# Kernel tuning notes

Hardware: AMD Instinct MI355X
Metric: run time of the kernel (lower is better)

The kernel has to match this reference:

```python
import jax, jax.numpy as jnp
import numpy as np

EPS = 1e-12  # F.normalize default eps


def _unfold(x, p):
    """im2col matching nn.Unfold(kernel_size=p, padding=p//2).
    x: (B,C,H,W) -> (B, C, p*p, H*W), kernel positions ordered row-major."""
    B, C, H, W = x.shape
    pad = p // 2
    xp = jnp.pad(x, ((0, 0), (0, 0), (pad, pad), (pad, pad)))
    shifts = [xp[:, :, i:i + H, j:j + W] for i in range(p) for j in range(p)]
    patches = jnp.stack(shifts, axis=2)  # (B,C,p*p,H,W)
    return patches.reshape(B, C, p * p, H * W)


def setup_inputs() -> dict:
    key = jax.random.key(0)
    k1, k2 = jax.random.split(key)
    B, C, H, W = 4, 128, 128, 128
    fe_lv = jax.random.normal(k1, (B, C, H, W), dtype=jnp.float32)
    fused_features = jax.random.normal(k2, (B, C, H, W), dtype=jnp.float32)
    return {"fe_lv": fe_lv, "fused_features": fused_features}


def reference(fe_lv, fused_features):
    p = 3
    B, C, H, W = fe_lv.shape
    K = p * p
    patches = _unfold(fused_features, p)          # (B,C,K,HW)
    fe_flat = fe_lv.reshape(B, C, H * W)          # (B,C,HW)

    # L2 normalize over channel dim (dim=1), clamped like F.normalize
    pn = patches / jnp.maximum(jnp.linalg.norm(patches, axis=1, keepdims=True), EPS)
    fn = fe_flat / jnp.maximum(jnp.linalg.norm(fe_flat, axis=1, keepdims=True), EPS)

    # cosine similarity per pixel over the K neighbors: (B,HW,K)
    cos = jnp.einsum('bckn,bcn->bnk', pn, fn)
    weights = jax.nn.softmax(cos, axis=-1)        # (B,HW,K)

    # weighted aggregation of (unnormalized) patches: (B,C,HW)
    refined = jnp.einsum('bnk,bckn->bcn', weights, patches)
    return refined.reshape(B, C, H, W) + fe_lv
```

## Files before the change

### kernel.cpp

```cpp
#include <hip/hip_runtime.h>
#include <math.h>

#define C_DIM 128
#define H_DIM 128
#define W_DIM 128
#define HW (H_DIM * W_DIM)
#define EPS_N 1e-12f
#define NT 512
#define NW 8
#define CPW 16
#define LD2(p) (*(const float2*)(p))

#define K1_PX 32
#define K1_NG 8
#define K1_CPG (C_DIM / K1_NG)
__global__ __launch_bounds__(256) void norms_fu(const float* __restrict__ fu,
                                                float* __restrict__ rn)
{
    __shared__ float part[K1_PX * 9];
    const int tid = threadIdx.x;
    const int px = tid & (K1_PX - 1);
    const int g = tid >> 5;
    const float* p = fu + (size_t)blockIdx.y * C_DIM * HW + (size_t)g * K1_CPG * HW
                     + blockIdx.x * K1_PX + px;
    float s = 0.f;
#pragma unroll
    for (int j = 0; j < K1_CPG; ++j) {
        const float v = p[(size_t)j * HW];
        s += v * v;
    }
    part[px * 9 + g] = s;
    __syncthreads();
    if (tid < K1_PX) {
        float t = 0.f;
#pragma unroll
        for (int gg = 0; gg < K1_NG; ++gg) t += part[tid * 9 + gg];
        rn[(size_t)blockIdx.y * HW + blockIdx.x * K1_PX + tid] =
            1.f / fmaxf(sqrtf(t), EPS_N);
    }
}

__global__ __launch_bounds__(NT) void asfr_main2(const float* __restrict__ fe,
                                                 const float* __restrict__ fu,
                                                 const float* __restrict__ rn,
                                                 float* __restrict__ out)
{
    __shared__ float part[NW][10][W_DIM];
    __shared__ float wl[9][W_DIM];
    __shared__ float n2r[3][W_DIM];

    const int tid = threadIdx.x;
    const int l   = tid & 63;
    const int wv  = tid >> 6;

    const int bid = blockIdx.x;
    const int cpx = gridDim.x >> 3;
    const int wb  = (bid & 7) * cpx + (bid >> 3);
    const int bz  = wb >> 7;
    const int row = wb & 127;

    const size_t imgbase = (size_t)bz * C_DIM * HW;
    const int c0   = wv * CPW;
    const int col0 = 2 * l;

    if (tid < 3 * W_DIM) {
        const int r = tid >> 7, c = tid & 127;
        const int nr = row + r - 1;
        float v = 1.f;
        if (nr >= 0 && nr < H_DIM) v = rn[(size_t)bz * HW + nr * W_DIM + c];
        n2r[r][c] = v;
    }

    const bool has_u = (row > 0), has_d = (row < H_DIM - 1);
    const int rup = has_u ? row - 1 : row;
    const int rdn = has_d ? row + 1 : row;

    const float* pfe = fe + imgbase + (size_t)c0 * HW + row * W_DIM + col0;
    const float* pfm = fu + imgbase + (size_t)c0 * HW + row * W_DIM + col0;
    const float* pfu = fu + imgbase + (size_t)c0 * HW + rup * W_DIM + col0;
    const float* pfd = fu + imgbase + (size_t)c0 * HW + rdn * W_DIM + col0;
    const float2 z2 = make_float2(0.f, 0.f);

    float2 dk[9];
#pragma unroll
    for (int k = 0; k < 9; ++k) dk[k] = z2;
    float2 fe2 = z2;

    auto acc3 = [&](const float2 f, const float2 v, const int r3) {
        float lft = __shfl_up(v.y, 1);   lft = (l == 0)  ? 0.f : lft;
        float rgt = __shfl_down(v.x, 1); rgt = (l == 63) ? 0.f : rgt;
        dk[r3+0].x += f.x * lft;  dk[r3+1].x += f.x * v.x;  dk[r3+2].x += f.x * v.y;
        dk[r3+0].y += f.y * v.x;  dk[r3+1].y += f.y * v.y;  dk[r3+2].y += f.y * rgt;
    };

#pragma unroll
    for (int jb = 0; jb < CPW / 2; ++jb) {
        const size_t offA = (size_t)(2 * jb) * HW;
        const size_t offB = offA + HW;
        float2 fA = LD2(pfe + offA); float2 uA = LD2(pfu + offA);
        float2 mA = LD2(pfm + offA); float2 dA = LD2(pfd + offA);
        float2 fB = LD2(pfe + offB); float2 uB = LD2(pfu + offB);
        float2 mB = LD2(pfm + offB); float2 dB = LD2(pfd + offB);
        if (!has_u) { uA = z2; uB = z2; }
        if (!has_d) { dA = z2; dB = z2; }
        fe2.x += fA.x * fA.x + fB.x * fB.x;
        fe2.y += fA.y * fA.y + fB.y * fB.y;
        acc3(fA, uA, 0); acc3(fA, mA, 3); acc3(fA, dA, 6);
        acc3(fB, uB, 0); acc3(fB, mB, 3); acc3(fB, dB, 6);
    }

#pragma unroll
    for (int k = 0; k < 9; ++k) *(float2*)&part[wv][k][col0] = dk[k];
    *(float2*)&part[wv][9][col0] = fe2;
    __syncthreads();

    if (tid < W_DIM) {
        const int px = tid;
        float dv[10];
#pragma unroll
        for (int k = 0; k < 10; ++k) {
            float s = 0.f;
#pragma unroll
            for (int w = 0; w < NW; ++w) s += part[w][k][px];
            dv[k] = s;
        }
        const float rfe = 1.f / fmaxf(sqrtf(dv[9]), EPS_N);
        float cs[9];
        float mx = -1e30f;
#pragma unroll
        for (int k = 0; k < 9; ++k) {
            const int di = k / 3, dj = k % 3;
            const int nr = row + di - 1;
            const int nc = px + dj - 1;
            const bool ok = (nr >= 0 && nr < H_DIM && nc >= 0 && nc < W_DIM);
            const int ncc = min(max(nc, 0), W_DIM - 1);
            const float cv = ok ? dv[k] * rfe * n2r[di][ncc] : 0.f;
            cs[k] = cv;
            mx = fmaxf(mx, cv);
        }
        float sum = 0.f;
#pragma unroll
        for (int k = 0; k < 9; ++k) { cs[k] = __expf(cs[k] - mx); sum += cs[k]; }
        const float is = 1.f / sum;
#pragma unroll
        for (int k = 0; k < 9; ++k) wl[k][px] = cs[k] * is;
    }
    __syncthreads();

    float2 w2[9];
#pragma unroll
    for (int k = 0; k < 9; ++k) w2[k] = *(const float2*)&wl[k][col0];

    auto agg3 = [&](float2& acc, const float2 v, const int r3) {
        float lft = __shfl_up(v.y, 1);   lft = (l == 0)  ? 0.f : lft;
        float rgt = __shfl_down(v.x, 1); rgt = (l == 63) ? 0.f : rgt;
        acc.x += w2[r3+0].x * lft  + w2[r3+1].x * v.x + w2[r3+2].x * v.y;
        acc.y += w2[r3+0].y * v.x  + w2[r3+1].y * v.y + w2[r3+2].y * rgt;
    };

    float* pout = out + imgbase + (size_t)c0 * HW + row * W_DIM + col0;
#pragma unroll
    for (int jb = 0; jb < CPW / 2; ++jb) {
        const size_t offA = (size_t)(2 * jb) * HW;
        const size_t offB = offA + HW;
        float2 fA = LD2(pfe + offA); float2 uA = LD2(pfu + offA);
        float2 mA = LD2(pfm + offA); float2 dA = LD2(pfd + offA);
        float2 fB = LD2(pfe + offB); float2 uB = LD2(pfu + offB);
        float2 mB = LD2(pfm + offB); float2 dB = LD2(pfd + offB);
        if (!has_u) { uA = z2; uB = z2; }
        if (!has_d) { dA = z2; dB = z2; }
        float2 accA = fA;
        float2 accB = fB;
        agg3(accA, uA, 0); agg3(accA, mA, 3); agg3(accA, dA, 6);
        agg3(accB, uB, 0); agg3(accB, mB, 3); agg3(accB, dB, 6);
        *(float2*)(pout + offA) = accA;
        *(float2*)(pout + offB) = accB;
    }
}

extern "C" void kernel_launch(void* const* d_in, const int* in_sizes, int n_in,
                              void* d_out, int out_size, void* d_ws, size_t ws_size,
                              hipStream_t stream) {
    const float* fe = (const float*)d_in[0];
    const float* fu = (const float*)d_in[1];
    float* out = (float*)d_out;
    float* rn = (float*)d_ws;
    const int B = in_sizes[0] / (C_DIM * HW);

    dim3 g1(HW / K1_PX, B);
    norms_fu<<<g1, 256, 0, stream>>>(fu, rn);

    dim3 g2(B * H_DIM);
    asfr_main2<<<g2, NT, 0, stream>>>(fe, fu, rn, out);
}
```

Baseline: 38.26 us.

## Split channel reduction across blocks and fuse patch norms into partial pass

Removes the separate norm kernel. A first kernel splits channels into four slices per row, each block computing partial dot products, fe norms and fu squared norms, and writes them to workspace. A second kernel sums the slice partials, derives neighbor-row inverse norms, computes the softmax weights and aggregates its channel slice. This quadruples the block count for better occupancy. In exchange it reads the inputs twice across separate kernels and adds workspace traffic for the partial sums.

```diff
diff --git a/kernel.cpp b/kernel.cpp
--- a/kernel.cpp
+++ b/kernel.cpp
@@ -6,48 +6,18 @@
 #define W_DIM 128
 #define HW (H_DIM * W_DIM)
 #define EPS_N 1e-12f
-#define NT 512
-#define NW 8
-#define CPW 16
+#define NSL 4
+#define CPS (C_DIM / NSL)
+#define CPWV 8
+#define NPL 11
+#define PS (NPL * W_DIM)
 #define LD2(p) (*(const float2*)(p))
 
-#define K1_PX 32
-#define K1_NG 8
-#define K1_CPG (C_DIM / K1_NG)
-__global__ __launch_bounds__(256) void norms_fu(const float* __restrict__ fu,
-                                                float* __restrict__ rn)
+__global__ __launch_bounds__(256) void k2_partial(const float* __restrict__ fe,
+                                                  const float* __restrict__ fu,
+                                                  float* __restrict__ pg)
 {
-    __shared__ float part[K1_PX * 9];
-    const int tid = threadIdx.x;
-    const int px = tid & (K1_PX - 1);
-    const int g = tid >> 5;
-    const float* p = fu + (size_t)blockIdx.y * C_DIM * HW + (size_t)g * K1_CPG * HW
-                     + blockIdx.x * K1_PX + px;
-    float s = 0.f;
-#pragma unroll
-    for (int j = 0; j < K1_CPG; ++j) {
-        const float v = p[(size_t)j * HW];
-        s += v * v;
-    }
-    part[px * 9 + g] = s;
-    __syncthreads();
-    if (tid < K1_PX) {
-        float t = 0.f;
-#pragma unroll
-        for (int gg = 0; gg < K1_NG; ++gg) t += part[tid * 9 + gg];
-        rn[(size_t)blockIdx.y * HW + blockIdx.x * K1_PX + tid] =
-            1.f / fmaxf(sqrtf(t), EPS_N);
-    }
-}
-
-__global__ __launch_bounds__(NT) void asfr_main2(const float* __restrict__ fe,
-                                                 const float* __restrict__ fu,
-                                                 const float* __restrict__ rn,
-                                                 float* __restrict__ out)
-{
-    __shared__ float part[NW][10][W_DIM];
-    __shared__ float wl[9][W_DIM];
-    __shared__ float n2r[3][W_DIM];
+    __shared__ float pl[4][PS];
 
     const int tid = threadIdx.x;
     const int l   = tid & 63;
@@ -56,20 +26,14 @@
     const int bid = blockIdx.x;
     const int cpx = gridDim.x >> 3;
     const int wb  = (bid & 7) * cpx + (bid >> 3);
-    const int bz  = wb >> 7;
-    const int row = wb & 127;
+    const int slice = wb & (NSL - 1);
+    const int RG  = wb >> 2;
+    const int bz  = RG >> 7;
+    const int row = RG & 127;
 
     const size_t imgbase = (size_t)bz * C_DIM * HW;
-    const int c0   = wv * CPW;
+    const int c0   = slice * CPS + wv * CPWV;
     const int col0 = 2 * l;
-
-    if (tid < 3 * W_DIM) {
-        const int r = tid >> 7, c = tid & 127;
-        const int nr = row + r - 1;
-        float v = 1.f;
-        if (nr >= 0 && nr < H_DIM) v = rn[(size_t)bz * HW + nr * W_DIM + c];
-        n2r[r][c] = v;
-    }
 
     const bool has_u = (row > 0), has_d = (row < H_DIM - 1);
     const int rup = has_u ? row - 1 : row;
@@ -84,7 +48,7 @@
     float2 dk[9];
 #pragma unroll
     for (int k = 0; k < 9; ++k) dk[k] = z2;
-    float2 fe2 = z2;
+    float2 fe2 = z2, s2 = z2;
 
     auto acc3 = [&](const float2 f, const float2 v, const int r3) {
         float lft = __shfl_up(v.y, 1);   lft = (l == 0)  ? 0.f : lft;
@@ -94,37 +58,68 @@
     };
 
 #pragma unroll
-    for (int jb = 0; jb < CPW / 2; ++jb) {
-        const size_t offA = (size_t)(2 * jb) * HW;
-        const size_t offB = offA + HW;
-        float2 fA = LD2(pfe + offA); float2 uA = LD2(pfu + offA);
-        float2 mA = LD2(pfm + offA); float2 dA = LD2(pfd + offA);
-        float2 fB = LD2(pfe + offB); float2 uB = LD2(pfu + offB);
-        float2 mB = LD2(pfm + offB); float2 dB = LD2(pfd + offB);
-        if (!has_u) { uA = z2; uB = z2; }
-        if (!has_d) { dA = z2; dB = z2; }
-        fe2.x += fA.x * fA.x + fB.x * fB.x;
-        fe2.y += fA.y * fA.y + fB.y * fB.y;
-        acc3(fA, uA, 0); acc3(fA, mA, 3); acc3(fA, dA, 6);
-        acc3(fB, uB, 0); acc3(fB, mB, 3); acc3(fB, dB, 6);
+    for (int j = 0; j < CPWV; ++j) {
+        const size_t off = (size_t)j * HW;
+        float2 f = LD2(pfe + off);
+        float2 u = LD2(pfu + off);
+        float2 m = LD2(pfm + off);
+        float2 d = LD2(pfd + off);
+        if (!has_u) u = z2;
+        if (!has_d) d = z2;
+        fe2.x += f.x * f.x; fe2.y += f.y * f.y;
+        s2.x  += m.x * m.x; s2.y  += m.y * m.y;
+        acc3(f, u, 0); acc3(f, m, 3); acc3(f, d, 6);
     }
 
 #pragma unroll
-    for (int k = 0; k < 9; ++k) *(float2*)&part[wv][k][col0] = dk[k];
-    *(float2*)&part[wv][9][col0] = fe2;
+    for (int k = 0; k < 9; ++k) *(float2*)&pl[wv][k * W_DIM + col0] = dk[k];
+    *(float2*)&pl[wv][9 * W_DIM + col0]  = fe2;
+    *(float2*)&pl[wv][10 * W_DIM + col0] = s2;
+    __syncthreads();
+
+    float* dst = pg + ((size_t)RG * NSL + slice) * PS;
+    for (int t = tid; t < PS; t += 256)
+        dst[t] = pl[0][t] + pl[1][t] + pl[2][t] + pl[3][t];
+}
+
+__global__ __launch_bounds__(256) void k3_agg(const float* __restrict__ fe,
+                                              const float* __restrict__ fu,
+                                              const float* __restrict__ pg,
+                                              float* __restrict__ out)
+{
+    __shared__ float dvs[10 * W_DIM];
+    __shared__ float n2r[3 * W_DIM];
+    __shared__ float wl[9][W_DIM];
+
+    const int tid = threadIdx.x;
+    const int l   = tid & 63;
+    const int wv  = tid >> 6;
+
+    const int bid = blockIdx.x;
+    const int cpx = gridDim.x >> 3;
+    const int wb  = (bid & 7) * cpx + (bid >> 3);
+    const int cg  = wb & (NSL - 1);
+    const int RG  = wb >> 2;
+    const int bz  = RG >> 7;
+    const int row = RG & 127;
+
+    {
+        const float* src = pg + (size_t)RG * NSL * PS;
+        for (int t = tid; t < 10 * W_DIM; t += 256)
+            dvs[t] = src[t] + src[PS + t] + src[2 * PS + t] + src[3 * PS + t];
+    }
+    for (int t = tid; t < 3 * W_DIM; t += 256) {
+        const int r = t >> 7, c = t & 127;
+        const int nrc = min(max(row + r - 1, 0), H_DIM - 1);
+        const float* nb = pg + ((size_t)(bz * H_DIM + nrc) * NSL) * PS + 10 * W_DIM;
+        const float s = nb[c] + nb[PS + c] + nb[2 * PS + c] + nb[3 * PS + c];
+        n2r[t] = 1.f / fmaxf(sqrtf(s), EPS_N);
+    }
     __syncthreads();
 
     if (tid < W_DIM) {
         const int px = tid;
-        float dv[10];
-#pragma unroll
-        for (int k = 0; k < 10; ++k) {
-            float s = 0.f;
-#pragma unroll
-            for (int w = 0; w < NW; ++w) s += part[w][k][px];
-            dv[k] = s;
-        }
-        const float rfe = 1.f / fmaxf(sqrtf(dv[9]), EPS_N);
+        const float rfe = 1.f / fmaxf(sqrtf(dvs[9 * W_DIM + px]), EPS_N);
         float cs[9];
         float mx = -1e30f;
 #pragma unroll
@@ -134,7 +129,7 @@
             const int nc = px + dj - 1;
             const bool ok = (nr >= 0 && nr < H_DIM && nc >= 0 && nc < W_DIM);
             const int ncc = min(max(nc, 0), W_DIM - 1);
-            const float cv = ok ? dv[k] * rfe * n2r[di][ncc] : 0.f;
+            const float cv = ok ? dvs[k * W_DIM + px] * rfe * n2r[di * W_DIM + ncc] : 0.f;
             cs[k] = cv;
             mx = fmaxf(mx, cv);
         }
@@ -147,6 +142,20 @@
     }
     __syncthreads();
 
+    const size_t imgbase = (size_t)bz * C_DIM * HW;
+    const int c0   = cg * CPS + wv * CPWV;
+    const int col0 = 2 * l;
+    const bool has_u = (row > 0), has_d = (row < H_DIM - 1);
+    const int rup = has_u ? row - 1 : row;
+    const int rdn = has_d ? row + 1 : row;
+
+    const float* pfe = fe + imgbase + (size_t)c0 * HW + row * W_DIM + col0;
+    const float* pfm = fu + imgbase + (size_t)c0 * HW + row * W_DIM + col0;
+    const float* pfu = fu + imgbase + (size_t)c0 * HW + rup * W_DIM + col0;
+    const float* pfd = fu + imgbase + (size_t)c0 * HW + rdn * W_DIM + col0;
+    float* pout = out + imgbase + (size_t)c0 * HW + row * W_DIM + col0;
+    const float2 z2 = make_float2(0.f, 0.f);
+
     float2 w2[9];
 #pragma unroll
     for (int k = 0; k < 9; ++k) w2[k] = *(const float2*)&wl[k][col0];
@@ -158,23 +167,18 @@
         acc.y += w2[r3+0].y * v.x  + w2[r3+1].y * v.y + w2[r3+2].y * rgt;
     };
 
-    float* pout = out + imgbase + (size_t)c0 * HW + row * W_DIM + col0;
 #pragma unroll
-    for (int jb = 0; jb < CPW / 2; ++jb) {
-        const size_t offA = (size_t)(2 * jb) * HW;
-        const size_t offB = offA + HW;
-        float2 fA = LD2(pfe + offA); float2 uA = LD2(pfu + offA);
-        float2 mA = LD2(pfm + offA); float2 dA = LD2(pfd + offA);
-        float2 fB = LD2(pfe + offB); float2 uB = LD2(pfu + offB);
-        float2 mB = LD2(pfm + offB); float2 dB = LD2(pfd + offB);
-        if (!has_u) { uA = z2; uB = z2; }
-        if (!has_d) { dA = z2; dB = z2; }
-        float2 accA = fA;
-        float2 accB = fB;
-        agg3(accA, uA, 0); agg3(accA, mA, 3); agg3(accA, dA, 6);
-        agg3(accB, uB, 0); agg3(accB, mB, 3); agg3(accB, dB, 6);
-        *(float2*)(pout + offA) = accA;
-        *(float2*)(pout + offB) = accB;
+    for (int j = 0; j < CPWV; ++j) {
+        const size_t off = (size_t)j * HW;
+        float2 f = LD2(pfe + off);
+        float2 u = LD2(pfu + off);
+        float2 m = LD2(pfm + off);
+        float2 d = LD2(pfd + off);
+        if (!has_u) u = z2;
+        if (!has_d) d = z2;
+        float2 acc = f;
+        agg3(acc, u, 0); agg3(acc, m, 3); agg3(acc, d, 6);
+        *(float2*)(pout + off) = acc;
     }
 }
 
@@ -184,12 +188,10 @@
     const float* fe = (const float*)d_in[0];
     const float* fu = (const float*)d_in[1];
     float* out = (float*)d_out;
-    float* rn = (float*)d_ws;
+    float* pg = (float*)d_ws;
     const int B = in_sizes[0] / (C_DIM * HW);
 
-    dim3 g1(HW / K1_PX, B);
-    norms_fu<<<g1, 256, 0, stream>>>(fu, rn);
-
-    dim3 g2(B * H_DIM);
-    asfr_main2<<<g2, NT, 0, stream>>>(fe, fu, rn, out);
+    dim3 g(B * H_DIM * NSL);
+    k2_partial<<<g, 256, 0, stream>>>(fe, fu, pg);
+    k3_agg<<<g, 256, 0, stream>>>(fe, fu, pg, out);
 }
```

Result: no change. 38.30 us (+0.1%).
